# Kernel optimization log

Measured on AMD Instinct MI355X. Metric: run time of the kernel, lower is better.

Reference implementation:

```python
import jax, jax.numpy as jnp
import numpy as np

TOKEN_SELF_ATTN_VALUE = -5e4  # reformer_pytorch constant for masking self-attention
BUCKET_SIZE = 64
N_HASHES = 4
HEADS = 8


def look_one_back(x):
    # concat each chunk with the previous chunk along the within-chunk axis (axis=2)
    prev = jnp.concatenate([x[:, -1:], x[:, :-1]], axis=1)
    return jnp.concatenate([prev, x], axis=2)


def lsh_attention(qk, v, rotations):
    # qk, v: (b*h, t, dh); rotations: (dh, n_hashes, n_buckets//2)
    bh, seqlen, dim = qk.shape
    n_buckets = seqlen // BUCKET_SIZE
    # --- LSH bucket hashing via random rotations ---
    rotated = jnp.einsum('btf,fhi->bhti', qk, rotations)            # (bh, H, t, nb/2)
    rotated = jnp.concatenate([rotated, -rotated], axis=-1)          # (bh, H, t, nb)
    buckets = jnp.argmax(rotated, axis=-1)                           # (bh, H, t)
    offsets = (jnp.arange(N_HASHES) * n_buckets)[None, :, None]
    buckets = (buckets + offsets).reshape(bh, N_HASHES * seqlen)
    # --- stable sort tokens by (bucket, position) ---
    ticker = jnp.arange(N_HASHES * seqlen)
    buckets_and_t = seqlen * buckets + (ticker % seqlen)[None, :]
    sticker = jnp.argsort(buckets_and_t, axis=-1)                    # sorted ticker
    undo_sort = jnp.argsort(sticker, axis=-1)
    st = sticker % seqlen                                            # original positions
    sqk = jnp.take_along_axis(qk, st[..., None], axis=1)
    sv = jnp.take_along_axis(v, st[..., None], axis=1)
    # --- chunk into n_hashes*n_buckets chunks of bucket_size tokens ---
    n_chunks = N_HASHES * n_buckets
    bq_t = st.reshape(bh, n_chunks, -1)
    bqk = sqk.reshape(bh, n_chunks, -1, dim)
    bv = sv.reshape(bh, n_chunks, -1, dim)
    bq = bqk
    bk = bqk / jnp.maximum(jnp.linalg.norm(bqk, axis=-1, keepdims=True), 1e-12)
    bk = look_one_back(bk)
    bv = look_one_back(bv)
    bkv_t = look_one_back(bq_t)
    # --- chunked attention with one-chunk lookback ---
    dots = jnp.einsum('bcie,bcje->bcij', bq, bk) * (dim ** -0.5)     # (bh, nc, bs, 2*bs)
    dots = jnp.where(bq_t[:, :, :, None] == bkv_t[:, :, None, :], TOKEN_SELF_ATTN_VALUE, dots)
    dots_lse = jax.nn.logsumexp(dots, axis=-1, keepdims=True)
    probs = jnp.exp(dots - dots_lse)
    bo = jnp.einsum('bcij,bcje->bcie', probs, bv)
    so = bo.reshape(bh, N_HASHES * seqlen, dim)
    slogits = dots_lse.reshape(bh, N_HASHES * seqlen)
    # --- unsort and combine hash rounds weighted by logsumexp ---
    o = jnp.take_along_axis(so, undo_sort[..., None], axis=1)
    logits = jnp.take_along_axis(slogits, undo_sort, axis=1)
    o = o.reshape(bh, N_HASHES, seqlen, dim)
    logits = logits.reshape(bh, N_HASHES, seqlen, 1)
    w = jnp.exp(logits - jax.nn.logsumexp(logits, axis=1, keepdims=True))
    return jnp.sum(o * w, axis=1)


def _forward(queries, Wqk, Wv, Wo, bo, rotations):
    B, N, C = queries.shape
    m = BUCKET_SIZE * 2
    if N % m != 0:  # fit_length: zero-pad to multiple of bucket_size*2 (static)
        pad = m - N % m
        x = jnp.concatenate([queries, jnp.zeros((B, pad, C), queries.dtype)], axis=1)
    else:
        x = queries
    T = x.shape[1]
    dh = C // HEADS
    qk = jnp.einsum('btc,cf->btf', x, Wqk).reshape(B, T, HEADS, dh).transpose(0, 2, 1, 3).reshape(B * HEADS, T, dh)
    v = jnp.einsum('btc,cf->btf', x, Wv).reshape(B, T, HEADS, dh).transpose(0, 2, 1, 3).reshape(B * HEADS, T, dh)
    out = lsh_attention(qk, v, rotations)
    out = out.reshape(B, HEADS, T, dh).transpose(0, 2, 1, 3).reshape(B, T, C)
    out = jnp.einsum('btc,cf->btf', out, Wo) + bo
    return out[:, :N]


def setup_inputs() -> dict:
    key = jax.random.key(0)
    ks = jax.random.split(key, 7)
    B, N, C = 4, 4096, 512
    dh = C // HEADS
    n_buckets = N // BUCKET_SIZE  # 64
    return {
        'queries': jax.random.normal(ks[0], (B, N, C), jnp.float32),
        'keys': jax.random.normal(ks[1], (B, N, C), jnp.float32),
        'values': jax.random.normal(ks[2], (B, N, C), jnp.float32),
        'attn_mask': jnp.zeros((1,), jnp.bool_),
        'tau': 1,
        'delta': 1,
        'Wqk': jax.random.normal(ks[3], (C, C), jnp.float32) / np.float32(np.sqrt(C)),
        'Wv': jax.random.normal(ks[4], (C, C), jnp.float32) / np.float32(np.sqrt(C)),
        'Wo': jax.random.normal(ks[5], (C, C), jnp.float32) / np.float32(np.sqrt(C)),
        'bo': jnp.zeros((C,), jnp.float32),
        'rotations': jax.random.normal(ks[6], (dh, N_HASHES, n_buckets // 2), jnp.float32),
    }


def reference(queries, keys, values, attn_mask, tau, delta, Wqk, Wv, Wo, bo, rotations):
    # keys/values/attn_mask/tau/delta are accepted but unused, matching the torch module
    return _forward(queries, Wqk, Wv, Wo, bo, rotations)
```

## Files before the change

### kernel.cpp

```cpp
#include <hip/hip_runtime.h>
#include <hip/hip_bf16.h>
#include <cstdint>
#include <cstddef>

#define LSEQ   4096
#define DHD    64
#define NHASH  4
#define CDIM   512
#define NBH    32
#define MROWS  16384
#define NCHUNK 256

typedef __attribute__((ext_vector_type(8))) short short8;
typedef __attribute__((ext_vector_type(4))) float f32x4;

__device__ inline uint32_t f2bf(float f) {
  uint32_t u = __float_as_uint(f);
  return (u + 0x7FFFu + ((u >> 16) & 1u)) >> 16;
}
__device__ inline float bf2f(uint32_t h) { return __uint_as_float(h << 16); }
__device__ inline void split2(float f, uint32_t& hi, uint32_t& lo) {
  hi = f2bf(f);
  lo = f2bf(f - bf2f(hi));
}
__device__ inline short8 ldsK(const uint16_t* p) {
  union { uint2 u[2]; short8 s; } t;
  t.u[0] = *reinterpret_cast<const uint2*>(p);
  t.u[1] = *reinterpret_cast<const uint2*>(p + 4);
  return t.s;
}

__global__ __launch_bounds__(256) void gemm_in_kernel(
    const float* __restrict__ X, const float* __restrict__ Wqk,
    const float* __restrict__ Wv, float* __restrict__ qk,
    uint16_t* __restrict__ qkhi, uint16_t* __restrict__ qklo,
    uint16_t* __restrict__ vhi, float* __restrict__ invn_g)
{
  const float* W = blockIdx.z ? Wv : Wqk;
  const int m0 = blockIdx.x * 128;
  const int n0 = blockIdx.y * 64;
  __shared__ float As[32][132];
  __shared__ float Bs[32][68];
  const int tid = threadIdx.x;
  const int r = tid >> 4, c = tid & 15;
  float acc[8][4];
#pragma unroll
  for (int i = 0; i < 8; i++)
#pragma unroll
    for (int j = 0; j < 4; j++) acc[i][j] = 0.f;

  const int arow = tid >> 3;
  const int ac4  = tid & 7;
  const int brow = tid >> 4;
  const int bc4  = tid & 15;

  for (int kb = 0; kb < CDIM; kb += 32) {
#pragma unroll
    for (int rr = 0; rr < 4; rr++) {
      int m = arow + rr * 32;
      float4 av = *reinterpret_cast<const float4*>(&X[(size_t)(m0 + m) * CDIM + kb + ac4 * 4]);
      As[ac4 * 4 + 0][m] = av.x;
      As[ac4 * 4 + 1][m] = av.y;
      As[ac4 * 4 + 2][m] = av.z;
      As[ac4 * 4 + 3][m] = av.w;
    }
#pragma unroll
    for (int rr = 0; rr < 2; rr++) {
      int kk = brow + rr * 16;
      *reinterpret_cast<float4*>(&Bs[kk][bc4 * 4]) =
          *reinterpret_cast<const float4*>(&W[(size_t)(kb + kk) * CDIM + n0 + bc4 * 4]);
    }
    __syncthreads();
#pragma unroll
    for (int k = 0; k < 32; k++) {
      float4 a0 = *reinterpret_cast<const float4*>(&As[k][r * 8]);
      float4 a1 = *reinterpret_cast<const float4*>(&As[k][r * 8 + 4]);
      float4 b  = *reinterpret_cast<const float4*>(&Bs[k][c * 4]);
      float am[8] = {a0.x, a0.y, a0.z, a0.w, a1.x, a1.y, a1.z, a1.w};
      float bn[4] = {b.x, b.y, b.z, b.w};
#pragma unroll
      for (int i = 0; i < 8; i++)
#pragma unroll
        for (int j = 0; j < 4; j++) acc[i][j] += am[i] * bn[j];
    }
    __syncthreads();
  }
  const int head = n0 >> 6;
  if (blockIdx.z == 0) {
#pragma unroll
    for (int ii = 0; ii < 8; ii++) {
      int m = m0 + r * 8 + ii;
      int b = m >> 12, t = m & 4095;
      size_t base = ((size_t)(b * 8 + head) * LSEQ + t) * DHD;
      float4 ov = {acc[ii][0], acc[ii][1], acc[ii][2], acc[ii][3]};
      *reinterpret_cast<float4*>(&qk[base + c * 4]) = ov;
      uint32_t h0, l0, h1, l1, h2, l2, h3, l3;
      split2(ov.x, h0, l0); split2(ov.y, h1, l1);
      split2(ov.z, h2, l2); split2(ov.w, h3, l3);
      uint2 hw = {(h1 << 16) | h0, (h3 << 16) | h2};
      uint2 lw = {(l1 << 16) | l0, (l3 << 16) | l2};
      *reinterpret_cast<uint2*>(&qkhi[base + c * 4]) = hw;
      *reinterpret_cast<uint2*>(&qklo[base + c * 4]) = lw;
      float ss = ov.x * ov.x + ov.y * ov.y + ov.z * ov.z + ov.w * ov.w;
      ss += __shfl_xor(ss, 1, 64);
      ss += __shfl_xor(ss, 2, 64);
      ss += __shfl_xor(ss, 4, 64);
      ss += __shfl_xor(ss, 8, 64);
      if (c == 0)
        invn_g[(size_t)(b * 8 + head) * LSEQ + t] = 1.0f / fmaxf(sqrtf(ss), 1e-12f);
    }
  } else {
#pragma unroll
    for (int ii = 0; ii < 8; ii++) {
      int m = m0 + r * 8 + ii;
      int b = m >> 12, t = m & 4095;
      size_t base = ((size_t)(b * 8 + head) * LSEQ + t) * DHD;
      uint32_t h0 = f2bf(acc[ii][0]), h1 = f2bf(acc[ii][1]);
      uint32_t h2 = f2bf(acc[ii][2]), h3 = f2bf(acc[ii][3]);
      uint2 hw = {(h1 << 16) | h0, (h3 << 16) | h2};
      *reinterpret_cast<uint2*>(&vhi[base + c * 4]) = hw;
    }
  }
}

__global__ __launch_bounds__(256) void hash_kernel(
    const float* __restrict__ qk, const float* __restrict__ rot,
    int* __restrict__ buckets)
{
  __shared__ float rotT[128][68];
  const int tid = threadIdx.x;
  for (int idx = tid; idx < 64 * 128; idx += 256) {
    int f = idx >> 7, hi = idx & 127;
    rotT[hi][f] = rot[idx];
  }
  __syncthreads();
  const int bh = blockIdx.y;
  const int t = blockIdx.x * 256 + tid;
  float4 row4[16];
  const float* src = &qk[((size_t)bh * LSEQ + t) * DHD];
#pragma unroll
  for (int i = 0; i < 16; i++) row4[i] = reinterpret_cast<const float4*>(src)[i];

  int* bout = &buckets[(size_t)bh * NHASH * LSEQ];
  for (int h = 0; h < NHASH; h++) {
    float rc[32];
    float best = -3.0e38f;
    int bidx = 0;
#pragma unroll 4
    for (int i = 0; i < 32; i++) {
      const float* rr = &rotT[h * 32 + i][0];
      float a = 0.f;
#pragma unroll
      for (int f4 = 0; f4 < 16; f4++) {
        float4 rv = reinterpret_cast<const float4*>(rr)[f4];
        a += row4[f4].x * rv.x + row4[f4].y * rv.y + row4[f4].z * rv.z + row4[f4].w * rv.w;
      }
      rc[i] = a;
      if (a > best) { best = a; bidx = i; }
    }
#pragma unroll
    for (int i = 0; i < 32; i++) {
      float nv = -rc[i];
      if (nv > best) { best = nv; bidx = 32 + i; }
    }
    bout[h * LSEQ + t] = bidx;
  }
}

__global__ __launch_bounds__(256) void sort_kernel(
    const int* __restrict__ buckets, int* __restrict__ st)
{
  __shared__ int hist[64][64];
  const int h = blockIdx.x, bh = blockIdx.y;
  const int tid = threadIdx.x;
  const int* bk = &buckets[((size_t)bh * NHASH + h) * LSEQ];

  for (int i = tid; i < 64 * 64; i += 256) (&hist[0][0])[i] = 0;
  __syncthreads();
  for (int t = tid; t < LSEQ; t += 256) {
    int b = bk[t];
    atomicAdd(&hist[t >> 6][b], 1);
  }
  __syncthreads();
  if (tid < 64) {
    int tot = 0;
    for (int s = 0; s < 64; s++) tot += hist[s][tid];
    int vsc = tot;
    for (int off = 1; off < 64; off <<= 1) {
      int nv = __shfl_up(vsc, off, 64);
      if (tid >= off) vsc += nv;
    }
    int run = h * LSEQ + (vsc - tot);
    for (int s = 0; s < 64; s++) {
      int tmp = hist[s][tid];
      hist[s][tid] = run;
      run += tmp;
    }
  }
  __syncthreads();
  const int wave = tid >> 6, lane = tid & 63;
  for (int si = 0; si < 16; si++) {
    int seg = wave * 16 + si;
    int pos = seg * 64 + lane;
    int b = bk[pos];
    int rank = 0;
    for (int k = 0; k < 64; k++) {
      int bb = __shfl(b, k, 64);
      rank += (bb == b && k < lane) ? 1 : 0;
    }
    int dest = hist[seg][b] + rank;
    st[(size_t)bh * (NHASH * LSEQ) + dest] = pos;
  }
}

__global__ __launch_bounds__(256) void attn_kernel(
    const uint16_t* __restrict__ qkhi, const uint16_t* __restrict__ qklo,
    const uint16_t* __restrict__ vhi, const float* __restrict__ invn_g,
    const int* __restrict__ st, uint16_t* __restrict__ o,
    float* __restrict__ lse_out)
{
  __shared__ __align__(16) uint8_t smem[53248];
  uint16_t* Khi  = (uint16_t*)smem;
  uint16_t* Klo  = Khi + 128 * 68;
  uint16_t* Vthi = (uint16_t*)(smem + 34816);
  float*    invn = (float*)(smem + 52224);
  int*      kpos = (int*)(smem + 52736);
  uint32_t* P32  = (uint32_t*)smem;

  const int cchunk = blockIdx.x, bh = blockIdx.y;
  const int tid = threadIdx.x;
  const int prev = (cchunk + NCHUNK - 1) & (NCHUNK - 1);
  const int* stb = &st[(size_t)bh * (NHASH * LSEQ)];
  const int h = cchunk >> 6;

  if (tid < 128) {
    int kp = (tid < 64) ? stb[prev * 64 + tid] : stb[cchunk * 64 + (tid - 64)];
    kpos[tid] = kp;
    invn[tid] = invn_g[(size_t)bh * LSEQ + kp];
  }
  __syncthreads();

  {
    const int d4 = tid & 15, rbase = tid >> 4;
    const uint16_t* qhb = qkhi + (size_t)bh * LSEQ * DHD;
    const uint16_t* qlb = qklo + (size_t)bh * LSEQ * DHD;
#pragma unroll
    for (int it = 0; it < 8; it++) {
      int row = rbase + it * 16;
      size_t src = (size_t)kpos[row] * DHD + d4 * 4;
      *reinterpret_cast<uint2*>(Khi + row * 68 + d4 * 4) =
          *reinterpret_cast<const uint2*>(qhb + src);
      *reinterpret_cast<uint2*>(Klo + row * 68 + d4 * 4) =
          *reinterpret_cast<const uint2*>(qlb + src);
    }
  }
  {
    const int d4 = tid & 15, jg0 = tid >> 4;
    const uint16_t* vb = vhi + (size_t)bh * LSEQ * DHD;
#pragma unroll
    for (int half = 0; half < 2; half++) {
      int jg = jg0 + half * 16;
      uint2 vr[4];
#pragma unroll
      for (int s = 0; s < 4; s++)
        vr[s] = *reinterpret_cast<const uint2*>(vb + (size_t)kpos[jg * 4 + s] * DHD + d4 * 4);
#pragma unroll
      for (int i = 0; i < 4; i++) {
        int d = d4 * 4 + i;
        uint32_t e0 = (((i & 2) ? vr[0].y : vr[0].x) >> ((i & 1) * 16)) & 0xffffu;
        uint32_t e1 = (((i & 2) ? vr[1].y : vr[1].x) >> ((i & 1) * 16)) & 0xffffu;
        uint32_t e2 = (((i & 2) ? vr[2].y : vr[2].x) >> ((i & 1) * 16)) & 0xffffu;
        uint32_t e3 = (((i & 2) ? vr[3].y : vr[3].x) >> ((i & 1) * 16)) & 0xffffu;
        uint2 outw = {e0 | (e1 << 16), e2 | (e3 << 16)};
        int cpr = (jg >> 1) ^ (d & 15);
        *reinterpret_cast<uint2*>(Vthi + d * 128 + cpr * 8 + (jg & 1) * 4) = outw;
      }
    }
  }
  __syncthreads();

  const int lane = tid & 63, w = tid >> 6;
  const int l16 = lane & 15, lg = lane >> 4;

  f32x4 acc[8];
#pragma unroll
  for (int nt = 0; nt < 8; nt++) acc[nt] = {0.f, 0.f, 0.f, 0.f};

#pragma unroll
  for (int ks = 0; ks < 2; ks++) {
    int aoff = (64 + w * 16 + l16) * 68 + ks * 32 + lg * 8;
    short8 a_hi = ldsK(Khi + aoff);
    short8 a_lo = ldsK(Klo + aoff);
#pragma unroll
    for (int nt = 0; nt < 8; nt++) {
      int boff = (nt * 16 + l16) * 68 + ks * 32 + lg * 8;
      short8 b_hi = ldsK(Khi + boff);
      short8 b_lo = ldsK(Klo + boff);
      acc[nt] = __builtin_amdgcn_mfma_f32_16x16x32_bf16(a_hi, b_hi, acc[nt], 0, 0, 0);
      acc[nt] = __builtin_amdgcn_mfma_f32_16x16x32_bf16(a_lo, b_hi, acc[nt], 0, 0, 0);
      acc[nt] = __builtin_amdgcn_mfma_f32_16x16x32_bf16(a_hi, b_lo, acc[nt], 0, 0, 0);
    }
  }

  float invc[8]; int kpc[8];
#pragma unroll
  for (int nt = 0; nt < 8; nt++) {
    invc[nt] = invn[nt * 16 + l16] * 0.125f;
    kpc[nt] = kpos[nt * 16 + l16];
  }
  float pll[4];
#pragma unroll
  for (int r = 0; r < 4; r++) {
    int q = w * 16 + lg * 4 + r;
    int qp = kpos[64 + q];
    float mm = -3.0e38f;
#pragma unroll
    for (int nt = 0; nt < 8; nt++) {
      float s = acc[nt][r] * invc[nt];
      if (qp == kpc[nt]) s = -5e4f;
      acc[nt][r] = s;
      mm = fmaxf(mm, s);
    }
    mm = fmaxf(mm, __shfl_xor(mm, 1, 64));
    mm = fmaxf(mm, __shfl_xor(mm, 2, 64));
    mm = fmaxf(mm, __shfl_xor(mm, 4, 64));
    mm = fmaxf(mm, __shfl_xor(mm, 8, 64));
    float ll = 0.f;
#pragma unroll
    for (int nt = 0; nt < 8; nt++) {
      float p = __expf(acc[nt][r] - mm);
      acc[nt][r] = p;
      ll += p;
    }
    ll += __shfl_xor(ll, 1, 64);
    ll += __shfl_xor(ll, 2, 64);
    ll += __shfl_xor(ll, 4, 64);
    ll += __shfl_xor(ll, 8, 64);
    if (l16 == 0)
      lse_out[(size_t)bh * (NHASH * LSEQ) + h * LSEQ + qp] = mm + __logf(ll);
    pll[r] = 1.0f / ll;
  }
  __syncthreads();

#pragma unroll
  for (int r = 0; r < 4; r++) {
    int q = w * 16 + lg * 4 + r;
#pragma unroll
    for (int nt = 0; nt < 8; nt++) {
      uint32_t phi, plo;
      split2(acc[nt][r], phi, plo);
      P32[q * 132 + nt * 16 + l16] = (plo << 16) | phi;
    }
  }

  f32x4 oacc[4];
#pragma unroll
  for (int nt = 0; nt < 4; nt++) oacc[nt] = {0.f, 0.f, 0.f, 0.f};

#pragma unroll
  for (int ks = 0; ks < 4; ks++) {
    const uint32_t* pr = P32 + (w * 16 + l16) * 132 + ks * 32 + lg * 8;
    uint4 ua = *reinterpret_cast<const uint4*>(pr);
    uint4 ub = *reinterpret_cast<const uint4*>(pr + 4);
    uint32_t u[8] = {ua.x, ua.y, ua.z, ua.w, ub.x, ub.y, ub.z, ub.w};
    union { uint32_t w4[4]; short8 s8; } ph, pl;
#pragma unroll
    for (int k2 = 0; k2 < 4; k2++) {
      ph.w4[k2] = (u[2 * k2] & 0xffffu) | (u[2 * k2 + 1] << 16);
      pl.w4[k2] = (u[2 * k2] >> 16) | (u[2 * k2 + 1] & 0xffff0000u);
    }
    const int cc = ks * 4 + lg;
#pragma unroll
    for (int nt = 0; nt < 4; nt++) {
      int voff = (nt * 16 + l16) * 128 + ((cc ^ l16) & 15) * 8;
      short8 v_hi = *reinterpret_cast<const short8*>(Vthi + voff);
      oacc[nt] = __builtin_amdgcn_mfma_f32_16x16x32_bf16(ph.s8, v_hi, oacc[nt], 0, 0, 0);
      oacc[nt] = __builtin_amdgcn_mfma_f32_16x16x32_bf16(pl.s8, v_hi, oacc[nt], 0, 0, 0);
    }
  }

  {
    uint16_t* ob = o + ((size_t)bh * (NHASH * LSEQ) + (size_t)h * LSEQ) * DHD;
#pragma unroll
    for (int r = 0; r < 4; r++) {
      int q = w * 16 + lg * 4 + r;
      int qp = kpos[64 + q];
      float s = pll[r];
#pragma unroll
      for (int nt = 0; nt < 4; nt++)
        ob[(size_t)qp * DHD + nt * 16 + l16] = (uint16_t)f2bf(oacc[nt][r] * s);
    }
  }
}

__global__ __launch_bounds__(256) void combine_kernel(
    const uint16_t* __restrict__ o, const float* __restrict__ lse,
    uint16_t* __restrict__ comb_hi, uint16_t* __restrict__ comb_lo)
{
  int gid = blockIdx.x * 4 + (threadIdx.x >> 6);
  int lane = threadIdx.x & 63;
  int bh = gid >> 12;
  int pos = gid & 4095;
  const float* lb = &lse[(size_t)bh * (NHASH * LSEQ) + pos];
  float l0 = lb[0], l1 = lb[LSEQ], l2 = lb[2 * LSEQ], l3 = lb[3 * LSEQ];
  float m = fmaxf(fmaxf(l0, l1), fmaxf(l2, l3));
  float w0 = __expf(l0 - m), w1 = __expf(l1 - m), w2 = __expf(l2 - m), w3 = __expf(l3 - m);
  float inv = 1.0f / (w0 + w1 + w2 + w3);
  const uint16_t* ob = &o[((size_t)bh * (NHASH * LSEQ) + pos) * DHD];
  float val = (w0 * bf2f(ob[lane]) + w1 * bf2f(ob[(size_t)LSEQ * DHD + lane]) +
               w2 * bf2f(ob[(size_t)2 * LSEQ * DHD + lane]) +
               w3 * bf2f(ob[(size_t)3 * LSEQ * DHD + lane])) * inv;
  int b = bh >> 3, head = bh & 7;
  size_t idx = ((size_t)(b * LSEQ + pos)) * CDIM + head * DHD + lane;
  uint32_t hi, lo;
  split2(val, hi, lo);
  comb_hi[idx] = (uint16_t)hi;
  comb_lo[idx] = (uint16_t)lo;
}

__global__ __launch_bounds__(256) void prep_wo_kernel(
    const float* __restrict__ Wo, uint16_t* __restrict__ th,
    uint16_t* __restrict__ tl)
{
  int idx = blockIdx.x * 256 + threadIdx.x;
  int k = idx >> 9, n = idx & 511;
  uint32_t hi, lo;
  split2(Wo[idx], hi, lo);
  th[n * 512 + k] = (uint16_t)hi;
  tl[n * 512 + k] = (uint16_t)lo;
}

__global__ __launch_bounds__(256) void gemm_out_kernel(
    const uint16_t* __restrict__ Ahi_g, const uint16_t* __restrict__ Alo_g,
    const uint16_t* __restrict__ Bhi_g, const uint16_t* __restrict__ Blo_g,
    const float* __restrict__ bias, float* __restrict__ out)
{
  __shared__ __align__(16) uint16_t Ah[128 * 40];
  __shared__ __align__(16) uint16_t Al[128 * 40];
  __shared__ __align__(16) uint16_t Bh[128 * 40];
  __shared__ __align__(16) uint16_t Bl[128 * 40];
  const int tid = threadIdx.x;
  const int m0 = blockIdx.x * 128, n0 = blockIdx.y * 128;
  const int lane = tid & 63, w = tid >> 6;
  const int l16 = lane & 15, lg = lane >> 4;
  const int mq = w >> 1, nq = w & 1;
  f32x4 acc[4][4];
#pragma unroll
  for (int i = 0; i < 4; i++)
#pragma unroll
    for (int j = 0; j < 4; j++) acc[i][j] = {0.f, 0.f, 0.f, 0.f};

  const int srow = tid >> 1, sh = tid & 1;
  for (int kb = 0; kb < CDIM; kb += 32) {
    {
      const uint4* sa_h = (const uint4*)(Ahi_g + (size_t)(m0 + srow) * CDIM + kb + sh * 16);
      const uint4* sa_l = (const uint4*)(Alo_g + (size_t)(m0 + srow) * CDIM + kb + sh * 16);
      const uint4* sb_h = (const uint4*)(Bhi_g + (size_t)(n0 + srow) * CDIM + kb + sh * 16);
      const uint4* sb_l = (const uint4*)(Blo_g + (size_t)(n0 + srow) * CDIM + kb + sh * 16);
      uint4* da_h = (uint4*)(Ah + srow * 40 + sh * 16);
      uint4* da_l = (uint4*)(Al + srow * 40 + sh * 16);
      uint4* db_h = (uint4*)(Bh + srow * 40 + sh * 16);
      uint4* db_l = (uint4*)(Bl + srow * 40 + sh * 16);
      da_h[0] = sa_h[0]; da_h[1] = sa_h[1];
      da_l[0] = sa_l[0]; da_l[1] = sa_l[1];
      db_h[0] = sb_h[0]; db_h[1] = sb_h[1];
      db_l[0] = sb_l[0]; db_l[1] = sb_l[1];
    }
    __syncthreads();
    short8 fa_h[4], fa_l[4], fb_h[4], fb_l[4];
#pragma unroll
    for (int mt = 0; mt < 4; mt++) {
      int ao = (mq * 64 + mt * 16 + l16) * 40 + lg * 8;
      fa_h[mt] = *reinterpret_cast<const short8*>(Ah + ao);
      fa_l[mt] = *reinterpret_cast<const short8*>(Al + ao);
    }
#pragma unroll
    for (int nt = 0; nt < 4; nt++) {
      int bo_ = (nq * 64 + nt * 16 + l16) * 40 + lg * 8;
      fb_h[nt] = *reinterpret_cast<const short8*>(Bh + bo_);
      fb_l[nt] = *reinterpret_cast<const short8*>(Bl + bo_);
    }
#pragma unroll
    for (int mt = 0; mt < 4; mt++)
#pragma unroll
      for (int nt = 0; nt < 4; nt++) {
        acc[mt][nt] = __builtin_amdgcn_mfma_f32_16x16x32_bf16(fa_h[mt], fb_h[nt], acc[mt][nt], 0, 0, 0);
        acc[mt][nt] = __builtin_amdgcn_mfma_f32_16x16x32_bf16(fa_l[mt], fb_h[nt], acc[mt][nt], 0, 0, 0);
        acc[mt][nt] = __builtin_amdgcn_mfma_f32_16x16x32_bf16(fa_h[mt], fb_l[nt], acc[mt][nt], 0, 0, 0);
      }
    __syncthreads();
  }
#pragma unroll
  for (int nt = 0; nt < 4; nt++) {
    int n = n0 + nq * 64 + nt * 16 + l16;
    float bv = bias[n];
#pragma unroll
    for (int mt = 0; mt < 4; mt++) {
#pragma unroll
      for (int rr = 0; rr < 4; rr++) {
        int m = m0 + mq * 64 + mt * 16 + lg * 4 + rr;
        out[(size_t)m * CDIM + n] = acc[mt][nt][rr] + bv;
      }
    }
  }
}

extern "C" void kernel_launch(void* const* d_in, const int* in_sizes, int n_in,
                              void* d_out, int out_size, void* d_ws, size_t ws_size,
                              hipStream_t stream) {
  (void)in_sizes; (void)n_in; (void)out_size; (void)ws_size;
  const float* X    = (const float*)d_in[0];
  const float* Wqk  = (const float*)d_in[6];
  const float* Wv   = (const float*)d_in[7];
  const float* Wo   = (const float*)d_in[8];
  const float* bo   = (const float*)d_in[9];
  const float* rot  = (const float*)d_in[10];

  uint8_t* W = (uint8_t*)d_ws;
  float*    qk      = (float*)(W + 0);
  uint16_t* obuf    = (uint16_t*)(W + 33554432);
  uint16_t* qkhi    = (uint16_t*)(W + 100663296);
  uint16_t* qklo    = (uint16_t*)(W + 117440512);
  uint16_t* vhi     = (uint16_t*)(W + 134217728);
  int*      buckets = (int*)(W + 150994944);
  int*      st      = (int*)(W + 153092096);
  float*    lse     = (float*)(W + 155189248);
  float*    invn_g  = (float*)(W + 157286400);
  uint16_t* woT_hi  = (uint16_t*)(W + 157810688);
  uint16_t* woT_lo  = (uint16_t*)(W + 158334976);
  uint16_t* comb_hi = (uint16_t*)(W + 0);
  uint16_t* comb_lo = (uint16_t*)(W + 16777216);

  hipLaunchKernelGGL(gemm_in_kernel, dim3(128, 8, 2), dim3(256), 0, stream,
                     X, Wqk, Wv, qk, qkhi, qklo, vhi, invn_g);
  hipLaunchKernelGGL(hash_kernel, dim3(16, 32), dim3(256), 0, stream,
                     qk, rot, buckets);
  hipLaunchKernelGGL(sort_kernel, dim3(4, 32), dim3(256), 0, stream,
                     buckets, st);
  hipLaunchKernelGGL(prep_wo_kernel, dim3(1024), dim3(256), 0, stream,
                     Wo, woT_hi, woT_lo);
  hipLaunchKernelGGL(attn_kernel, dim3(256, 32), dim3(256), 0, stream,
                     qkhi, qklo, vhi, invn_g, st, obuf, lse);
  hipLaunchKernelGGL(combine_kernel, dim3(32768), dim3(256), 0, stream,
                     obuf, lse, comb_hi, comb_lo);
  hipLaunchKernelGGL(gemm_out_kernel, dim3(128, 4), dim3(256), 0, stream,
                     comb_hi, comb_lo, woT_hi, woT_lo, bo, (float*)d_out);
}
```

Baseline: 514.5 us.

## Move V projection to split-bf16 MFMA GEMM and pack QK FMAs

Splits the fused QK/V input projection into two kernels. The V projection now runs on bf16 MFMA using three-term hi/lo splits, with new prep kernels that split X and transpose-split Wv. The QK GEMM keeps FP32 FMA but uses 2-wide float vectors so the compiler can emit packed FMAs. This adds two extra launches, extra traffic for the bf16 copies of X, and narrow 2-byte scattered stores for V.

```diff
diff --git a/kernel.cpp b/kernel.cpp
--- a/kernel.cpp
+++ b/kernel.cpp
@@ -13,6 +13,7 @@
 
 typedef __attribute__((ext_vector_type(8))) short short8;
 typedef __attribute__((ext_vector_type(4))) float f32x4;
+typedef __attribute__((ext_vector_type(2))) float f32x2;
 
 __device__ inline uint32_t f2bf(float f) {
   uint32_t u = __float_as_uint(f);
@@ -30,24 +31,65 @@
   return t.s;
 }
 
-__global__ __launch_bounds__(256) void gemm_in_kernel(
+__global__ __launch_bounds__(256) void prep_x_kernel(
+    const float* __restrict__ X, uint16_t* __restrict__ X0,
+    uint16_t* __restrict__ X1)
+{
+  size_t i = ((size_t)blockIdx.x * 256 + threadIdx.x) * 4;
+  float4 v = *reinterpret_cast<const float4*>(X + i);
+  uint32_t h[4], l[4];
+#pragma unroll
+  for (int j = 0; j < 4; j++) split2((&v.x)[j], h[j], l[j]);
+  uint2 hw = {(h[1] << 16) | h[0], (h[3] << 16) | h[2]};
+  uint2 lw = {(l[1] << 16) | l[0], (l[3] << 16) | l[2]};
+  *reinterpret_cast<uint2*>(X0 + i) = hw;
+  *reinterpret_cast<uint2*>(X1 + i) = lw;
+}
+
+__global__ __launch_bounds__(256) void prep_wv_kernel(
+    const float* __restrict__ Wv,
+    uint16_t* __restrict__ v0, uint16_t* __restrict__ v1)
+{
+  __shared__ float Ts[32][33];
+  const int tid = threadIdx.x;
+  const int k0 = blockIdx.x * 32, n0 = blockIdx.y * 32;
+#pragma unroll
+  for (int i = 0; i < 4; i++) {
+    int flat = i * 256 + tid;
+    int r = flat >> 5, c = flat & 31;
+    Ts[r][c] = Wv[(size_t)(k0 + r) * 512 + n0 + c];
+  }
+  __syncthreads();
+#pragma unroll
+  for (int i = 0; i < 4; i++) {
+    int flat = i * 256 + tid;
+    int nr = flat >> 5, kc = flat & 31;
+    uint32_t h, l;
+    split2(Ts[kc][nr], h, l);
+    size_t idx = (size_t)(n0 + nr) * 512 + k0 + kc;
+    v0[idx] = (uint16_t)h;
+    v1[idx] = (uint16_t)l;
+  }
+}
+
+__global__ __launch_bounds__(256) void gemm_qk_kernel(
     const float* __restrict__ X, const float* __restrict__ Wqk,
-    const float* __restrict__ Wv, float* __restrict__ qk,
-    uint16_t* __restrict__ qkhi, uint16_t* __restrict__ qklo,
-    uint16_t* __restrict__ vhi, float* __restrict__ invn_g)
-{
-  const float* W = blockIdx.z ? Wv : Wqk;
+    float* __restrict__ qk, uint16_t* __restrict__ qkhi,
+    uint16_t* __restrict__ qklo, float* __restrict__ invn_g)
+{
+  const float* W = Wqk;
   const int m0 = blockIdx.x * 128;
   const int n0 = blockIdx.y * 64;
   __shared__ float As[32][132];
   __shared__ float Bs[32][68];
   const int tid = threadIdx.x;
   const int r = tid >> 4, c = tid & 15;
-  float acc[8][4];
-#pragma unroll
-  for (int i = 0; i < 8; i++)
-#pragma unroll
-    for (int j = 0; j < 4; j++) acc[i][j] = 0.f;
+  f32x2 acc2[8][2];
+#pragma unroll
+  for (int i = 0; i < 8; i++) {
+    acc2[i][0] = {0.f, 0.f};
+    acc2[i][1] = {0.f, 0.f};
+  }
 
   const int arow = tid >> 3;
   const int ac4  = tid & 7;
@@ -77,48 +119,100 @@
       float4 a1 = *reinterpret_cast<const float4*>(&As[k][r * 8 + 4]);
       float4 b  = *reinterpret_cast<const float4*>(&Bs[k][c * 4]);
       float am[8] = {a0.x, a0.y, a0.z, a0.w, a1.x, a1.y, a1.z, a1.w};
-      float bn[4] = {b.x, b.y, b.z, b.w};
-#pragma unroll
-      for (int i = 0; i < 8; i++)
-#pragma unroll
-        for (int j = 0; j < 4; j++) acc[i][j] += am[i] * bn[j];
+      f32x2 b01 = {b.x, b.y};
+      f32x2 b23 = {b.z, b.w};
+#pragma unroll
+      for (int i = 0; i < 8; i++) {
+        f32x2 av = {am[i], am[i]};
+        acc2[i][0] += av * b01;
+        acc2[i][1] += av * b23;
+      }
     }
     __syncthreads();
   }
   const int head = n0 >> 6;
-  if (blockIdx.z == 0) {
-#pragma unroll
-    for (int ii = 0; ii < 8; ii++) {
-      int m = m0 + r * 8 + ii;
-      int b = m >> 12, t = m & 4095;
-      size_t base = ((size_t)(b * 8 + head) * LSEQ + t) * DHD;
-      float4 ov = {acc[ii][0], acc[ii][1], acc[ii][2], acc[ii][3]};
-      *reinterpret_cast<float4*>(&qk[base + c * 4]) = ov;
-      uint32_t h0, l0, h1, l1, h2, l2, h3, l3;
-      split2(ov.x, h0, l0); split2(ov.y, h1, l1);
-      split2(ov.z, h2, l2); split2(ov.w, h3, l3);
-      uint2 hw = {(h1 << 16) | h0, (h3 << 16) | h2};
-      uint2 lw = {(l1 << 16) | l0, (l3 << 16) | l2};
-      *reinterpret_cast<uint2*>(&qkhi[base + c * 4]) = hw;
-      *reinterpret_cast<uint2*>(&qklo[base + c * 4]) = lw;
-      float ss = ov.x * ov.x + ov.y * ov.y + ov.z * ov.z + ov.w * ov.w;
-      ss += __shfl_xor(ss, 1, 64);
-      ss += __shfl_xor(ss, 2, 64);
-      ss += __shfl_xor(ss, 4, 64);
-      ss += __shfl_xor(ss, 8, 64);
-      if (c == 0)
-        invn_g[(size_t)(b * 8 + head) * LSEQ + t] = 1.0f / fmaxf(sqrtf(ss), 1e-12f);
-    }
-  } else {
-#pragma unroll
-    for (int ii = 0; ii < 8; ii++) {
-      int m = m0 + r * 8 + ii;
-      int b = m >> 12, t = m & 4095;
-      size_t base = ((size_t)(b * 8 + head) * LSEQ + t) * DHD;
-      uint32_t h0 = f2bf(acc[ii][0]), h1 = f2bf(acc[ii][1]);
-      uint32_t h2 = f2bf(acc[ii][2]), h3 = f2bf(acc[ii][3]);
-      uint2 hw = {(h1 << 16) | h0, (h3 << 16) | h2};
-      *reinterpret_cast<uint2*>(&vhi[base + c * 4]) = hw;
+#pragma unroll
+  for (int ii = 0; ii < 8; ii++) {
+    int m = m0 + r * 8 + ii;
+    int b = m >> 12, t = m & 4095;
+    size_t base = ((size_t)(b * 8 + head) * LSEQ + t) * DHD;
+    float4 ov = {acc2[ii][0][0], acc2[ii][0][1], acc2[ii][1][0], acc2[ii][1][1]};
+    *reinterpret_cast<float4*>(&qk[base + c * 4]) = ov;
+    uint32_t h0, l0, h1, l1, h2, l2, h3, l3;
+    split2(ov.x, h0, l0); split2(ov.y, h1, l1);
+    split2(ov.z, h2, l2); split2(ov.w, h3, l3);
+    uint2 hw = {(h1 << 16) | h0, (h3 << 16) | h2};
+    uint2 lw = {(l1 << 16) | l0, (l3 << 16) | l2};
+    *reinterpret_cast<uint2*>(&qkhi[base + c * 4]) = hw;
+    *reinterpret_cast<uint2*>(&qklo[base + c * 4]) = lw;
+    float ss = ov.x * ov.x + ov.y * ov.y + ov.z * ov.z + ov.w * ov.w;
+    ss += __shfl_xor(ss, 1, 64);
+    ss += __shfl_xor(ss, 2, 64);
+    ss += __shfl_xor(ss, 4, 64);
+    ss += __shfl_xor(ss, 8, 64);
+    if (c == 0)
+      invn_g[(size_t)(b * 8 + head) * LSEQ + t] = 1.0f / fmaxf(sqrtf(ss), 1e-12f);
+  }
+}
+
+__global__ __launch_bounds__(512) void gemm_v_mfma_kernel(
+    const uint16_t* __restrict__ X0g, const uint16_t* __restrict__ X1g,
+    const uint16_t* __restrict__ Wv0, const uint16_t* __restrict__ Wv1,
+    uint16_t* __restrict__ vhi)
+{
+  __shared__ __align__(16) uint16_t Xs[2 * 128 * 40];
+  __shared__ __align__(16) uint16_t Ws[2 * 128 * 40];
+  const int tid = threadIdx.x;
+  const int m0 = blockIdx.x * 128;
+  const int n0 = blockIdx.y * 128;
+  const int lane = tid & 63, w = tid >> 6;
+  const int l16 = lane & 15, lg = lane >> 4;
+
+  f32x4 acc[8];
+#pragma unroll
+  for (int nt = 0; nt < 8; nt++) acc[nt] = {0.f, 0.f, 0.f, 0.f};
+
+  const int srow = tid >> 3;
+  const int sch = (tid & 7) * 4;
+
+  for (int kb = 0; kb < CDIM; kb += 32) {
+#pragma unroll
+    for (int i = 0; i < 4; i++) {
+      int p = i >> 1;
+      int row = (i & 1) * 64 + srow;
+      const uint16_t* xg = (p == 0) ? X0g : X1g;
+      const uint16_t* wg = (p == 0) ? Wv0 : Wv1;
+      *reinterpret_cast<uint2*>(Xs + p * 5120 + row * 40 + sch) =
+          *reinterpret_cast<const uint2*>(xg + (size_t)(m0 + row) * 512 + kb + sch);
+      *reinterpret_cast<uint2*>(Ws + p * 5120 + row * 40 + sch) =
+          *reinterpret_cast<const uint2*>(wg + (size_t)(n0 + row) * 512 + kb + sch);
+    }
+    __syncthreads();
+
+    const int abase = (w * 16 + l16) * 40 + lg * 8;
+    short8 a0 = *reinterpret_cast<const short8*>(Xs + abase);
+    short8 a1 = *reinterpret_cast<const short8*>(Xs + 5120 + abase);
+#pragma unroll
+    for (int nt = 0; nt < 8; nt++) {
+      int bbase = (nt * 16 + l16) * 40 + lg * 8;
+      short8 b0 = *reinterpret_cast<const short8*>(Ws + bbase);
+      short8 b1 = *reinterpret_cast<const short8*>(Ws + 5120 + bbase);
+      acc[nt] = __builtin_amdgcn_mfma_f32_16x16x32_bf16(a0, b0, acc[nt], 0, 0, 0);
+      acc[nt] = __builtin_amdgcn_mfma_f32_16x16x32_bf16(a1, b0, acc[nt], 0, 0, 0);
+      acc[nt] = __builtin_amdgcn_mfma_f32_16x16x32_bf16(a0, b1, acc[nt], 0, 0, 0);
+    }
+    __syncthreads();
+  }
+
+#pragma unroll
+  for (int rr = 0; rr < 4; rr++) {
+    int mg = m0 + w * 16 + lg * 4 + rr;
+    int b = mg >> 12, t = mg & 4095;
+#pragma unroll
+    for (int nt = 0; nt < 8; nt++) {
+      int head = (n0 >> 6) + (nt >> 2);
+      size_t base = ((size_t)(b * 8 + head) * LSEQ + t) * DHD + (nt & 3) * 16 + l16;
+      vhi[base] = (uint16_t)f2bf(acc[nt][rr]);
     }
   }
 }
@@ -528,11 +622,21 @@
   float*    invn_g  = (float*)(W + 157286400);
   uint16_t* woT_hi  = (uint16_t*)(W + 157810688);
   uint16_t* woT_lo  = (uint16_t*)(W + 158334976);
+  uint16_t* wvT0    = (uint16_t*)(W + 158859264);
+  uint16_t* wvT1    = (uint16_t*)(W + 159383552);
+  uint16_t* x0      = (uint16_t*)(W + 33554432);
+  uint16_t* x1      = (uint16_t*)(W + 50331648);
   uint16_t* comb_hi = (uint16_t*)(W + 0);
   uint16_t* comb_lo = (uint16_t*)(W + 16777216);
 
-  hipLaunchKernelGGL(gemm_in_kernel, dim3(128, 8, 2), dim3(256), 0, stream,
-                     X, Wqk, Wv, qk, qkhi, qklo, vhi, invn_g);
+  hipLaunchKernelGGL(prep_x_kernel, dim3(8192), dim3(256), 0, stream,
+                     X, x0, x1);
+  hipLaunchKernelGGL(prep_wv_kernel, dim3(16, 16), dim3(256), 0, stream,
+                     Wv, wvT0, wvT1);
+  hipLaunchKernelGGL(gemm_qk_kernel, dim3(128, 8), dim3(256), 0, stream,
+                     X, Wqk, qk, qkhi, qklo, invn_g);
+  hipLaunchKernelGGL(gemm_v_mfma_kernel, dim3(128, 4), dim3(512), 0, stream,
+                     x0, x1, wvT0, wvT1, vhi);
   hipLaunchKernelGGL(hash_kernel, dim3(16, 32), dim3(256), 0, stream,
                      qk, rot, buckets);
   hipLaunchKernelGGL(sort_kernel, dim3(4, 32), dim3(256), 0, stream,
```

After: 460.1 us. -10.6%, faster.
